# Kernel tuning notes

Hardware: AMD Instinct MI355X
Metric: run time of the kernel (lower is better)

## Reference

```python
import jax, jax.numpy as jnp
import numpy as np

B, Q, K, H = 32, 256, 256, 128

def setup_inputs() -> dict:
    key = jax.random.key(0)
    k1, k2, k3, k4 = jax.random.split(key, 4)
    queries = jax.random.normal(k1, (B, Q, H), dtype=jnp.float32)
    keys = jax.random.normal(k2, (B, K, H), dtype=jnp.float32)
    values = jax.random.normal(k3, (B, K, H), dtype=jnp.float32)
    # nn.Linear(hidden_size, 1, bias=False) weight, stored as a length-H vector
    w = jax.random.normal(k4, (H,), dtype=jnp.float32) * (1.0 / np.sqrt(H))
    return {"queries": queries, "keys": keys, "values": values, "w": w}


def reference(queries, keys, values, w):
    # Y: [B, Q, K, H] broadcast sum, then tanh
    Y = jnp.tanh(queries[:, :, None, :] + keys[:, None, :, :])
    # scores: [B, Q, K] = Y @ w
    scores = jnp.einsum("bqkh,h->bqk", Y, w)
    attn = jax.nn.softmax(scores, axis=-1)
    # output: [B, Q, Hv]
    return jnp.einsum("bqk,bkv->bqv", attn, values)
```

## Files before the change

kernel.cpp:

```cpp
#include <hip/hip_runtime.h>
#include <math.h>

#define C2 2.8853900817779268f

__global__ __launch_bounds__(512) void addattn_kernel(
    const float* __restrict__ q_g, const float* __restrict__ k_g,
    const float* __restrict__ v_g, const float* __restrict__ w_g,
    float* __restrict__ out)
{
    __shared__ float kbuf[32768];
    __shared__ float sB[8192];

    const int tid  = threadIdx.x;
    const int lane = tid & 63;
    const int wv   = __builtin_amdgcn_readfirstlane(tid >> 6);

    const int xcd = blockIdx.x & 7;
    const int sub = blockIdx.x >> 3;
    const int b   = (xcd << 2) + (sub >> 3);
    const int qr0 = ((sub & 7) << 5) + (wv << 2);

    float* strip = sB + (wv << 10);

    if (lane < 32) *(float4*)&strip[512 + (lane << 2)] = ((const float4*)w_g)[lane];
    {
        const float* qb = q_g + (size_t)(b * 256 + qr0) * 128;
        #pragma unroll
        for (int j = 0; j < 2; ++j) {
            int f = lane + (j << 6);
            int r = f >> 5, c = f & 31;
            float4 qv = *(const float4*)(qb + (r << 7) + (c << 2));
            float4 E;
            E.x = __builtin_amdgcn_exp2f(C2 * qv.x);
            E.y = __builtin_amdgcn_exp2f(C2 * qv.y);
            E.z = __builtin_amdgcn_exp2f(C2 * qv.z);
            E.w = __builtin_amdgcn_exp2f(C2 * qv.w);
            *(float4*)&strip[(r << 7) + (c << 2)] = E;
        }
    }

    {
        const float4* kg4 = (const float4*)(k_g + (size_t)b * 32768);
        #pragma unroll
        for (int j = 0; j < 16; ++j) {
            int f = tid + (j << 9);
            float4 kv = kg4[f];
            int k = f >> 5, g = f & 31;
            float4 E;
            E.x = __builtin_amdgcn_exp2f(C2 * kv.x);
            E.y = __builtin_amdgcn_exp2f(C2 * kv.y);
            E.z = __builtin_amdgcn_exp2f(C2 * kv.z);
            E.w = __builtin_amdgcn_exp2f(C2 * kv.w);
            int rot = ((k & 63) + g) & 63;
            *(float4*)&kbuf[((k >> 6) << 13) + (g << 8) + (rot << 2)] = E;
        }
    }
    __syncthreads();

    float s[4][4];
    #pragma unroll
    for (int t = 0; t < 4; ++t)
        #pragma unroll
        for (int r = 0; r < 4; ++r) s[t][r] = 0.f;

    #pragma unroll 4
    for (int g = 0; g < 32; ++g) {
        float4 w4 = *(const float4*)&strip[512 + (g << 2)];
        float4 e0 = *(const float4*)&strip[g << 2];
        float4 e1 = *(const float4*)&strip[128 + (g << 2)];
        float4 e2 = *(const float4*)&strip[256 + (g << 2)];
        float4 e3 = *(const float4*)&strip[384 + (g << 2)];
        const int rot = (((lane + g) & 63) << 2) + (g << 8);
        #pragma unroll
        for (int t = 0; t < 4; ++t) {
            float4 k4 = *(const float4*)&kbuf[(t << 13) + rot];
            #define RB(E, S)                                                   \
            {                                                                  \
                float d0 = fmaf(E.x, k4.x, 1.f), d1 = fmaf(E.y, k4.y, 1.f);    \
                float d2 = fmaf(E.z, k4.z, 1.f), d3 = fmaf(E.w, k4.w, 1.f);    \
                float P01 = d0 * d1, P23 = d2 * d3;                            \
                float N01 = fmaf(w4.x, d1, w4.y * d0);                         \
                float N23 = fmaf(w4.z, d3, w4.w * d2);                         \
                float num = fmaf(N01, P23, N23 * P01);                         \
                S = fmaf(num, __builtin_amdgcn_rcpf(P01 * P23), S);            \
            }
            RB(e0, s[t][0])
            RB(e1, s[t][1])
            RB(e2, s[t][2])
            RB(e3, s[t][3])
            #undef RB
        }
    }

    #pragma unroll
    for (int r = 0; r < 4; ++r) {
        float x0 = -C2 * s[0][r], x1 = -C2 * s[1][r];
        float x2 = -C2 * s[2][r], x3 = -C2 * s[3][r];
        float m = fmaxf(fmaxf(x0, x1), fmaxf(x2, x3));
        #pragma unroll
        for (int off = 32; off; off >>= 1) m = fmaxf(m, __shfl_xor(m, off));
        float e0 = __builtin_amdgcn_exp2f(x0 - m);
        float e1 = __builtin_amdgcn_exp2f(x1 - m);
        float e2 = __builtin_amdgcn_exp2f(x2 - m);
        float e3 = __builtin_amdgcn_exp2f(x3 - m);
        float sum = (e0 + e1) + (e2 + e3);
        #pragma unroll
        for (int off = 32; off; off >>= 1) sum += __shfl_xor(sum, off);
        float inv = __builtin_amdgcn_rcpf(sum);
        strip[(r << 8) + lane]       = e0 * inv;
        strip[(r << 8) + 64 + lane]  = e1 * inv;
        strip[(r << 8) + 128 + lane] = e2 * inv;
        strip[(r << 8) + 192 + lane] = e3 * inv;
    }

    float2 o0, o1, o2, o3;
    o0.x = o0.y = o1.x = o1.y = 0.f;
    o2.x = o2.y = o3.x = o3.y = 0.f;
    const float2* vp = (const float2*)(v_g + (size_t)b * 32768) + lane;
    #pragma unroll 4
    for (int j4 = 0; j4 < 64; ++j4) {
        float4 a0 = *(const float4*)(strip + (j4 << 2));
        float4 a1 = *(const float4*)(strip + 256 + (j4 << 2));
        float4 a2 = *(const float4*)(strip + 512 + (j4 << 2));
        float4 a3 = *(const float4*)(strip + 768 + (j4 << 2));
        #pragma unroll
        for (int i = 0; i < 4; ++i) {
            float2 v2 = vp[((j4 << 2) + i) << 6];
            float c0 = (&a0.x)[i], c1 = (&a1.x)[i], c2 = (&a2.x)[i], c3 = (&a3.x)[i];
            o0.x = fmaf(c0, v2.x, o0.x); o0.y = fmaf(c0, v2.y, o0.y);
            o1.x = fmaf(c1, v2.x, o1.x); o1.y = fmaf(c1, v2.y, o1.y);
            o2.x = fmaf(c2, v2.x, o2.x); o2.y = fmaf(c2, v2.y, o2.y);
            o3.x = fmaf(c3, v2.x, o3.x); o3.y = fmaf(c3, v2.y, o3.y);
        }
    }

    float* ob = out + (size_t)(b * 256 + qr0) * 128 + (lane << 1);
    *(float2*)(ob)       = o0;
    *(float2*)(ob + 128) = o1;
    *(float2*)(ob + 256) = o2;
    *(float2*)(ob + 384) = o3;
}

extern "C" void kernel_launch(void* const* d_in, const int* in_sizes, int n_in,
                              void* d_out, int out_size, void* d_ws, size_t ws_size,
                              hipStream_t stream) {
    const float* q = (const float*)d_in[0];
    const float* k = (const float*)d_in[1];
    const float* v = (const float*)d_in[2];
    const float* w = (const float*)d_in[3];
    float* out = (float*)d_out;
    addattn_kernel<<<256, 512, 0, stream>>>(q, k, v, w, out);
}
```

Measured before the change: 42.71 us.

## Store exp(2K) in bf16 LDS and halve block size for two blocks per CU

Stores the exponentiated keys in shared memory as packed bf16 pairs instead of fp32, halving the key buffer to 64 KB. Blocks shrink to 256 threads (16 query rows) and the grid doubles to 512, with launch bounds asking for two blocks per CU. The aim is higher occupancy and lower LDS read traffic in the score loop. In exchange each block recomputes the key exponentials, so that work doubles, and bf16 rounding of exp(2k) costs score precision.

Measured after the change: 44.20 us. +3.5%, slower.

```diff
diff --git a/kernel.cpp b/kernel.cpp
--- a/kernel.cpp
+++ b/kernel.cpp
@@ -1,24 +1,29 @@
 #include <hip/hip_runtime.h>
+#include <hip/hip_bf16.h>
 #include <math.h>
 
 #define C2 2.8853900817779268f
 
-__global__ __launch_bounds__(512) void addattn_kernel(
+__device__ __forceinline__ unsigned int pack_bf16(float a, float b) {
+    __hip_bfloat162 h = __float22bfloat162_rn(float2{a, b});
+    return *reinterpret_cast<unsigned int*>(&h);
+}
+
+__global__ __launch_bounds__(256, 2) void addattn_kernel(
     const float* __restrict__ q_g, const float* __restrict__ k_g,
     const float* __restrict__ v_g, const float* __restrict__ w_g,
     float* __restrict__ out)
 {
-    __shared__ float kbuf[32768];
-    __shared__ float sB[8192];
+    __shared__ unsigned int kbuf[16384];
+    __shared__ float sB[4096];
 
     const int tid  = threadIdx.x;
     const int lane = tid & 63;
     const int wv   = __builtin_amdgcn_readfirstlane(tid >> 6);
 
-    const int xcd = blockIdx.x & 7;
-    const int sub = blockIdx.x >> 3;
-    const int b   = (xcd << 2) + (sub >> 3);
-    const int qr0 = ((sub & 7) << 5) + (wv << 2);
+    const int o   = ((blockIdx.x & 7) << 6) + (blockIdx.x >> 3);
+    const int b   = o >> 4;
+    const int qr0 = ((o & 15) << 4) + (wv << 2);
 
     float* strip = sB + (wv << 10);
 
@@ -41,18 +46,21 @@
 
     {
         const float4* kg4 = (const float4*)(k_g + (size_t)b * 32768);
-        #pragma unroll
-        for (int j = 0; j < 16; ++j) {
-            int f = tid + (j << 9);
+        #pragma unroll 8
+        for (int j = 0; j < 32; ++j) {
+            int f = tid + (j << 8);
             float4 kv = kg4[f];
             int k = f >> 5, g = f & 31;
-            float4 E;
-            E.x = __builtin_amdgcn_exp2f(C2 * kv.x);
-            E.y = __builtin_amdgcn_exp2f(C2 * kv.y);
-            E.z = __builtin_amdgcn_exp2f(C2 * kv.z);
-            E.w = __builtin_amdgcn_exp2f(C2 * kv.w);
+            float e0 = __builtin_amdgcn_exp2f(C2 * kv.x);
+            float e1 = __builtin_amdgcn_exp2f(C2 * kv.y);
+            float e2 = __builtin_amdgcn_exp2f(C2 * kv.z);
+            float e3 = __builtin_amdgcn_exp2f(C2 * kv.w);
+            uint2 p;
+            p.x = pack_bf16(e0, e1);
+            p.y = pack_bf16(e2, e3);
             int rot = ((k & 63) + g) & 63;
-            *(float4*)&kbuf[((k >> 6) << 13) + (g << 8) + (rot << 2)] = E;
+            int pair = ((((k >> 6) << 5) | g) << 6) + rot;
+            *(uint2*)&kbuf[pair << 1] = p;
         }
     }
     __syncthreads();
@@ -70,14 +78,18 @@
         float4 e1 = *(const float4*)&strip[128 + (g << 2)];
         float4 e2 = *(const float4*)&strip[256 + (g << 2)];
         float4 e3 = *(const float4*)&strip[384 + (g << 2)];
-        const int rot = (((lane + g) & 63) << 2) + (g << 8);
+        const int rot = (lane + g) & 63;
         #pragma unroll
         for (int t = 0; t < 4; ++t) {
-            float4 k4 = *(const float4*)&kbuf[(t << 13) + rot];
+            uint2 kp = *(const uint2*)&kbuf[(((((t << 5) | g) << 6) + rot) << 1)];
+            float k0 = __uint_as_float(kp.x << 16);
+            float k1 = __uint_as_float(kp.x & 0xFFFF0000u);
+            float k2 = __uint_as_float(kp.y << 16);
+            float k3 = __uint_as_float(kp.y & 0xFFFF0000u);
             #define RB(E, S)                                                   \
             {                                                                  \
-                float d0 = fmaf(E.x, k4.x, 1.f), d1 = fmaf(E.y, k4.y, 1.f);    \
-                float d2 = fmaf(E.z, k4.z, 1.f), d3 = fmaf(E.w, k4.w, 1.f);    \
+                float d0 = fmaf(E.x, k0, 1.f), d1 = fmaf(E.y, k1, 1.f);        \
+                float d2 = fmaf(E.z, k2, 1.f), d3 = fmaf(E.w, k3, 1.f);        \
                 float P01 = d0 * d1, P23 = d2 * d3;                            \
                 float N01 = fmaf(w4.x, d1, w4.y * d0);                         \
                 float N23 = fmaf(w4.z, d3, w4.w * d2);                         \
@@ -149,5 +161,5 @@
     const float* v = (const float*)d_in[2];
     const float* w = (const float*)d_in[3];
     float* out = (float*)d_out;
-    addattn_kernel<<<256, 512, 0, stream>>>(q, k, v, w, out);
+    addattn_kernel<<<512, 256, 0, stream>>>(q, k, v, w, out);
 }
```
